# Optimization experiments

Measured on AMD Instinct MI355X. Metric: run time of the kernel, lower is better.

## Reference

```python
import jax, jax.numpy as jnp
import numpy as np

B, I, H = 32768, 1024, 1024

def _xavier(key, shape):
    fan_out, fan_in = shape
    limit = float(np.sqrt(6.0 / (fan_in + fan_out)))
    return jax.random.uniform(key, shape, jnp.float32, -limit, limit)

def setup_inputs() -> dict:
    key = jax.random.key(0)
    ks = jax.random.split(key, 8)
    return {
        "x": jax.random.normal(ks[0], (B, I), jnp.float32),
        "h": jax.random.normal(ks[1], (B, H), jnp.float32),
        "weight_ir": _xavier(ks[2], (H, I)),
        "weight_hr": _xavier(ks[3], (H, H)),
        "weight_iz": _xavier(ks[4], (H, I)),
        "weight_hz": _xavier(ks[5], (H, H)),
        "weight_in": _xavier(ks[6], (H, I)),
        "weight_hn": _xavier(ks[7], (H, H)),
        "bias_ir": jnp.zeros((H,), jnp.float32),
        "bias_hr": jnp.zeros((H,), jnp.float32),
        "bias_iz": jnp.zeros((H,), jnp.float32),
        "bias_hz": jnp.zeros((H,), jnp.float32),
        "bias_in": jnp.zeros((H,), jnp.float32),
        "bias_hn": jnp.zeros((H,), jnp.float32),
    }

def reference(x, h, weight_ir, weight_hr, weight_iz, weight_hz, weight_in, weight_hn,
              bias_ir, bias_hr, bias_iz, bias_hz, bias_in, bias_hn):
    # Fuse the 3 input-side and 3 hidden-side GEMMs into two concatenated GEMMs
    # (same math as 6 separate F.linear calls).
    Wi = jnp.concatenate([weight_ir, weight_iz, weight_in], axis=0)  # [3H, I]
    Wh = jnp.concatenate([weight_hr, weight_hz, weight_hn], axis=0)  # [3H, H]
    bi = jnp.concatenate([bias_ir, bias_iz, bias_in])
    bh = jnp.concatenate([bias_hr, bias_hz, bias_hn])
    gi = x @ Wi.T + bi   # [B, 3H]
    gh = h @ Wh.T + bh   # [B, 3H]
    Hd = weight_hr.shape[0]
    ir, iz, inn = gi[:, :Hd], gi[:, Hd:2*Hd], gi[:, 2*Hd:]
    hr, hz, hn = gh[:, :Hd], gh[:, Hd:2*Hd], gh[:, 2*Hd:]
    r = jax.nn.sigmoid(ir + hr)
    z = jax.nn.sigmoid(iz + hz)
    n = jnp.tanh(inn + r * hn)
    return (1.0 - z) * n + z * h
```

## Files before the change

kernel.cpp:

```cpp
#include <hip/hip_runtime.h>
#include <hip/hip_bf16.h>


#define B_ROWS 32768
#define KD     1024
#define HD     1024

#define BM 128
#define BN 64
#define BK 32

typedef __bf16 bf16_t;
typedef __bf16 bf16x8 __attribute__((ext_vector_type(8)));
typedef __bf16 bf16x4 __attribute__((ext_vector_type(4)));
typedef float  f32x4  __attribute__((ext_vector_type(4)));

#define XT_BYTES  67108864ull
#define WT_OFF   134217728ull
#define WS_NEEDED 146800640ull

#define X_SLOTS 4194304
#define W_BASE_SLOT 8388608
#define TOTAL_SLOTS 9175040

__device__ __forceinline__ float sigm_f(float v) { return 1.0f / (1.0f + __expf(-v)); }
__device__ __forceinline__ float tanh_f(float v) { return 2.0f / (1.0f + __expf(-2.0f * v)) - 1.0f; }

__device__ __forceinline__ bf16x4 cvt4(f32x4 v) {
    bf16x4 r;
    r[0] = (bf16_t)v[0]; r[1] = (bf16_t)v[1];
    r[2] = (bf16_t)v[2]; r[3] = (bf16_t)v[3];
    return r;
}

__device__ __forceinline__ void glds16(const void* g, void* l) {
    __builtin_amdgcn_global_load_lds(
        (const __attribute__((address_space(1))) void*)g,
        (__attribute__((address_space(3))) void*)l, 16, 0, 0);
}

struct WPtrs { const float* p[6]; };

__global__ void __launch_bounds__(256)
cvt_kernel(const float* __restrict__ x, const float* __restrict__ h,
           WPtrs wp, bf16_t* __restrict__ ws)
{
    int sid = blockIdx.x * 256 + threadIdx.x;
    if (sid >= TOTAL_SLOTS) return;

    const float* src;
    if (sid < W_BASE_SLOT) {
        const float* base = (sid < X_SLOTS) ? x : h;
        int s2   = sid & (X_SLOTS - 1);
        int tile = s2 >> 9;
        int c    = s2 & 511;
        int row  = c >> 2, s = c & 3;
        int mt   = tile >> 5, kt = tile & 31;
        int ks   = s ^ ((row >> 1) & 3);
        src = base + (size_t)(mt * 128 + row) * KD + kt * 32 + ks * 8;
    } else {
        int s2   = sid - W_BASE_SLOT;
        int tile = s2 / 1536;
        int c    = s2 % 1536;
        int g    = c >> 8;
        int cc   = c & 255;
        int row  = cc >> 2, s = cc & 3;
        int nt   = tile >> 5, kt = tile & 31;
        int ks   = s ^ ((row >> 1) & 3);
        src = wp.p[g] + (size_t)(nt * 64 + row) * KD + kt * 32 + ks * 8;
    }
    f32x4 a = *(const f32x4*)src;
    f32x4 b = *(const f32x4*)(src + 4);
    bf16x8 o;
    o[0]=(bf16_t)a[0]; o[1]=(bf16_t)a[1]; o[2]=(bf16_t)a[2]; o[3]=(bf16_t)a[3];
    o[4]=(bf16_t)b[0]; o[5]=(bf16_t)b[1]; o[6]=(bf16_t)b[2]; o[7]=(bf16_t)b[3];
    *(bf16x8*)(ws + (size_t)sid * 8) = o;
}

__global__ void __launch_bounds__(256, 2)
gru_mfma_kernel(const bf16_t* __restrict__ xt, const bf16_t* __restrict__ ht,
                const bf16_t* __restrict__ wt,
                const float* __restrict__ h,
                const float* __restrict__ b_ir, const float* __restrict__ b_hr,
                const float* __restrict__ b_iz, const float* __restrict__ b_hz,
                const float* __restrict__ b_in, const float* __restrict__ b_hn,
                float* __restrict__ out)
{
    __shared__ __align__(16) char smem[2][40960];

    const int tid  = threadIdx.x;
    const int lane = tid & 63;
    const int wid  = tid >> 6;
    const int wr   = wid >> 1;
    const int wc   = wid & 1;

    const int nblk = HD / BN;
    const int bidN = blockIdx.x % nblk;
    const int bidM = blockIdx.x / nblk;
    const int rowBase = bidM * BM;
    const int colBase = bidN * BN;

    const char* xcb = (const char*)xt + (size_t)bidM * 32 * 8192;
    const char* hcb = (const char*)ht + (size_t)bidM * 32 * 8192;
    const char* wcb = (const char*)wt + (size_t)bidN * 32 * 24576;

    const f32x4 vzero = {0.f, 0.f, 0.f, 0.f};
    f32x4 accR[4][2], accZ[4][2], accIN[4][2], accHN[4][2];
    #pragma unroll
    for (int m = 0; m < 4; ++m)
        #pragma unroll
        for (int n = 0; n < 2; ++n) {
            accR[m][n] = vzero; accZ[m][n] = vzero;
            accIN[m][n] = vzero; accHN[m][n] = vzero;
        }

    const int fr  = lane & 15;
    const int sl  = lane >> 4;
    const int f   = (fr >> 1) & 3;
    const int col = ((sl ^ f) << 4);
    int aoff[4], boff[2];
    #pragma unroll
    for (int m = 0; m < 4; ++m) aoff[m] = (wr * 64 + m * 16 + fr) * 64 + col;
    #pragma unroll
    for (int n = 0; n < 2; ++n) boff[n] = (wc * 32 + n * 16 + fr) * 64 + col;

    auto STAGE = [&](int buf, int kt) {
        const char* xc  = xcb + (size_t)kt * 8192;
        const char* hc  = hcb + (size_t)kt * 8192;
        const char* wc2 = wcb + (size_t)kt * 24576;
        char* s = smem[buf];
        #pragma unroll
        for (int i = 0; i < 2; ++i) {
            int off = wid * 2048 + i * 1024;
            glds16(xc + off + lane * 16, s + off);
            glds16(hc + off + lane * 16, s + 8192 + off);
        }
        #pragma unroll
        for (int j = 0; j < 6; ++j) {
            int off = wid * 6144 + j * 1024;
            glds16(wc2 + off + lane * 16, s + 16384 + off);
        }
    };

    auto COMPUTE = [&](const char* s) {
        bf16x8 xa[4], ha[4];
        #pragma unroll
        for (int m = 0; m < 4; ++m) {
            xa[m] = *(const bf16x8*)(s + aoff[m]);
            ha[m] = *(const bf16x8*)(s + 8192 + aoff[m]);
        }
        bf16x8 wb[6][2];
        #pragma unroll
        for (int g = 0; g < 6; ++g)
            #pragma unroll
            for (int n = 0; n < 2; ++n)
                wb[g][n] = *(const bf16x8*)(s + 16384 + g * 4096 + boff[n]);

        #pragma unroll
        for (int m = 0; m < 4; ++m) {
            #pragma unroll
            for (int n = 0; n < 2; ++n) {
                accR[m][n]  = __builtin_amdgcn_mfma_f32_16x16x32_bf16(xa[m], wb[0][n], accR[m][n], 0, 0, 0);
                accR[m][n]  = __builtin_amdgcn_mfma_f32_16x16x32_bf16(ha[m], wb[1][n], accR[m][n], 0, 0, 0);
                accZ[m][n]  = __builtin_amdgcn_mfma_f32_16x16x32_bf16(xa[m], wb[2][n], accZ[m][n], 0, 0, 0);
                accZ[m][n]  = __builtin_amdgcn_mfma_f32_16x16x32_bf16(ha[m], wb[3][n], accZ[m][n], 0, 0, 0);
                accIN[m][n] = __builtin_amdgcn_mfma_f32_16x16x32_bf16(xa[m], wb[4][n], accIN[m][n], 0, 0, 0);
                accHN[m][n] = __builtin_amdgcn_mfma_f32_16x16x32_bf16(ha[m], wb[5][n], accHN[m][n], 0, 0, 0);
            }
        }
    };

    STAGE(0, 0);

    for (int kt = 0; kt < 31; ++kt) {
        STAGE((kt + 1) & 1, kt + 1);
        asm volatile("s_waitcnt vmcnt(10)" ::: "memory");
        __builtin_amdgcn_s_barrier();
        __builtin_amdgcn_sched_barrier(0);
        COMPUTE(smem[kt & 1]);
        __builtin_amdgcn_sched_barrier(0);
        __builtin_amdgcn_s_barrier();
    }
    asm volatile("s_waitcnt vmcnt(0)" ::: "memory");
    __builtin_amdgcn_s_barrier();
    __builtin_amdgcn_sched_barrier(0);
    COMPUTE(smem[1]);

    const int rq = (lane >> 4) * 4;
    float br[2], bz[2], bi[2], bh[2];
    #pragma unroll
    for (int n = 0; n < 2; ++n) {
        int c = colBase + wc * 32 + n * 16 + fr;
        br[n] = b_ir[c] + b_hr[c];
        bz[n] = b_iz[c] + b_hz[c];
        bi[n] = b_in[c];
        bh[n] = b_hn[c];
    }
    #pragma unroll
    for (int m = 0; m < 4; ++m) {
        #pragma unroll
        for (int n = 0; n < 2; ++n) {
            int gc = colBase + wc * 32 + n * 16 + fr;
            #pragma unroll
            for (int j = 0; j < 4; ++j) {
                int gr = rowBase + wr * 64 + m * 16 + rq + j;
                float rv = sigm_f(accR[m][n][j] + br[n]);
                float zv = sigm_f(accZ[m][n][j] + bz[n]);
                float nv = tanh_f(accIN[m][n][j] + bi[n] + rv * (accHN[m][n][j] + bh[n]));
                float hv = h[(size_t)gr * HD + gc];
                out[(size_t)gr * HD + gc] = (1.0f - zv) * nv + zv * hv;
            }
        }
    }
}

#define PK 40
__global__ void __launch_bounds__(256, 2)
gru_fused_kernel(const float* __restrict__ x,  const float* __restrict__ h,
                 const float* __restrict__ w_ir, const float* __restrict__ w_hr,
                 const float* __restrict__ w_iz, const float* __restrict__ w_hz,
                 const float* __restrict__ w_in, const float* __restrict__ w_hn,
                 const float* __restrict__ b_ir, const float* __restrict__ b_hr,
                 const float* __restrict__ b_iz, const float* __restrict__ b_hz,
                 const float* __restrict__ b_in, const float* __restrict__ b_hn,
                 float* __restrict__ out)
{
    __shared__ __align__(16) bf16_t xs[BM][PK];
    __shared__ __align__(16) bf16_t hs[BM][PK];
    __shared__ __align__(16) bf16_t ws[6][BN][PK];

    const int tid  = threadIdx.x;
    const int lane = tid & 63;
    const int wid  = tid >> 6;
    const int wr   = wid >> 1;
    const int wc   = wid & 1;

    const int nblk = HD / BN;
    const int bidN = blockIdx.x % nblk;
    const int bidM = blockIdx.x / nblk;
    const int rowBase = bidM * BM;
    const int colBase = bidN * BN;

    const float* wptr[6] = { w_ir, w_hr, w_iz, w_hz, w_in, w_hn };

    int sr[4], sc[4];
    #pragma unroll
    for (int i = 0; i < 4; ++i) {
        int idx = tid + i * 256;
        sr[i] = idx >> 3;
        sc[i] = (idx & 7) * 4;
    }
    int xoff[4];
    #pragma unroll
    for (int i = 0; i < 4; ++i) xoff[i] = (rowBase + sr[i]) * KD + sc[i];
    int woff[2];
    #pragma unroll
    for (int i = 0; i < 2; ++i) woff[i] = (colBase + sr[i]) * KD + sc[i];

    const f32x4 vzero = {0.f, 0.f, 0.f, 0.f};
    f32x4 accR[4][2], accZ[4][2], accIN[4][2], accHN[4][2];
    #pragma unroll
    for (int m = 0; m < 4; ++m)
        #pragma unroll
        for (int n = 0; n < 2; ++n) {
            accR[m][n] = vzero; accZ[m][n] = vzero;
            accIN[m][n] = vzero; accHN[m][n] = vzero;
        }

    const int fr = lane & 15;
    const int ko = (lane >> 4) * 8;

    for (int k0 = 0; k0 < KD; k0 += BK) {
        __syncthreads();
        #pragma unroll
        for (int i = 0; i < 4; ++i) {
            f32x4 vx = *(const f32x4*)&x[xoff[i] + k0];
            f32x4 vh = *(const f32x4*)&h[xoff[i] + k0];
            *(bf16x4*)&xs[sr[i]][sc[i]] = cvt4(vx);
            *(bf16x4*)&hs[sr[i]][sc[i]] = cvt4(vh);
        }
        #pragma unroll
        for (int g = 0; g < 6; ++g) {
            #pragma unroll
            for (int i = 0; i < 2; ++i) {
                f32x4 vw = *(const f32x4*)&wptr[g][woff[i] + k0];
                *(bf16x4*)&ws[g][sr[i]][sc[i]] = cvt4(vw);
            }
        }
        __syncthreads();

        bf16x8 xa[4], ha[4];
        #pragma unroll
        for (int m = 0; m < 4; ++m) {
            xa[m] = *(const bf16x8*)&xs[wr * 64 + m * 16 + fr][ko];
            ha[m] = *(const bf16x8*)&hs[wr * 64 + m * 16 + fr][ko];
        }
        bf16x8 wb[6][2];
        #pragma unroll
        for (int g = 0; g < 6; ++g)
            #pragma unroll
            for (int n = 0; n < 2; ++n)
                wb[g][n] = *(const bf16x8*)&ws[g][wc * 32 + n * 16 + fr][ko];

        #pragma unroll
        for (int m = 0; m < 4; ++m) {
            #pragma unroll
            for (int n = 0; n < 2; ++n) {
                accR[m][n]  = __builtin_amdgcn_mfma_f32_16x16x32_bf16(xa[m], wb[0][n], accR[m][n], 0, 0, 0);
                accR[m][n]  = __builtin_amdgcn_mfma_f32_16x16x32_bf16(ha[m], wb[1][n], accR[m][n], 0, 0, 0);
                accZ[m][n]  = __builtin_amdgcn_mfma_f32_16x16x32_bf16(xa[m], wb[2][n], accZ[m][n], 0, 0, 0);
                accZ[m][n]  = __builtin_amdgcn_mfma_f32_16x16x32_bf16(ha[m], wb[3][n], accZ[m][n], 0, 0, 0);
                accIN[m][n] = __builtin_amdgcn_mfma_f32_16x16x32_bf16(xa[m], wb[4][n], accIN[m][n], 0, 0, 0);
                accHN[m][n] = __builtin_amdgcn_mfma_f32_16x16x32_bf16(ha[m], wb[5][n], accHN[m][n], 0, 0, 0);
            }
        }
    }

    const int rq = (lane >> 4) * 4;
    float br[2], bz[2], bi[2], bh[2];
    #pragma unroll
    for (int n = 0; n < 2; ++n) {
        int c = colBase + wc * 32 + n * 16 + fr;
        br[n] = b_ir[c] + b_hr[c];
        bz[n] = b_iz[c] + b_hz[c];
        bi[n] = b_in[c];
        bh[n] = b_hn[c];
    }
    #pragma unroll
    for (int m = 0; m < 4; ++m) {
        #pragma unroll
        for (int n = 0; n < 2; ++n) {
            int gc = colBase + wc * 32 + n * 16 + fr;
            #pragma unroll
            for (int j = 0; j < 4; ++j) {
                int gr = rowBase + wr * 64 + m * 16 + rq + j;
                float rv = sigm_f(accR[m][n][j] + br[n]);
                float zv = sigm_f(accZ[m][n][j] + bz[n]);
                float nv = tanh_f(accIN[m][n][j] + bi[n] + rv * (accHN[m][n][j] + bh[n]));
                float hv = h[gr * HD + gc];
                out[gr * HD + gc] = (1.0f - zv) * nv + zv * hv;
            }
        }
    }
}

extern "C" void kernel_launch(void* const* d_in, const int* in_sizes, int n_in,
                              void* d_out, int out_size, void* d_ws, size_t ws_size,
                              hipStream_t stream) {
    const float* x    = (const float*)d_in[0];
    const float* h    = (const float*)d_in[1];
    const float* w_ir = (const float*)d_in[2];
    const float* w_hr = (const float*)d_in[3];
    const float* w_iz = (const float*)d_in[4];
    const float* w_hz = (const float*)d_in[5];
    const float* w_in = (const float*)d_in[6];
    const float* w_hn = (const float*)d_in[7];
    const float* b_ir = (const float*)d_in[8];
    const float* b_hr = (const float*)d_in[9];
    const float* b_iz = (const float*)d_in[10];
    const float* b_hz = (const float*)d_in[11];
    const float* b_in = (const float*)d_in[12];
    const float* b_hn = (const float*)d_in[13];
    float* out = (float*)d_out;

    if (ws_size >= WS_NEEDED) {
        bf16_t* ws = (bf16_t*)d_ws;
        WPtrs wp;
        wp.p[0] = w_ir; wp.p[1] = w_hr; wp.p[2] = w_iz;
        wp.p[3] = w_hz; wp.p[4] = w_in; wp.p[5] = w_hn;
        cvt_kernel<<<(TOTAL_SLOTS + 255) / 256, 256, 0, stream>>>(x, h, wp, ws);

        const bf16_t* xt = ws;
        const bf16_t* ht = ws + XT_BYTES / 2;
        const bf16_t* wt = ws + WT_OFF / 2;
        dim3 grid((B_ROWS / BM) * (HD / BN));
        gru_mfma_kernel<<<grid, 256, 0, stream>>>(
            xt, ht, wt, h, b_ir, b_hr, b_iz, b_hz, b_in, b_hn, out);
    } else {
        dim3 grid((B_ROWS / BM) * (HD / BN));
        gru_fused_kernel<<<grid, 256, 0, stream>>>(
            x, h, w_ir, w_hr, w_iz, w_hz, w_in, w_hn,
            b_ir, b_hr, b_iz, b_hz, b_in, b_hn, out);
    }
}
```

Measured before the change: 473.2 us.

## Split K-step into three interleaved load/MFMA phases with priority and block swizzle

Reworks the main K loop so the next tile's global-to-LDS loads are spread across three compute phases (R, Z, N gates), each phase reading only its weight fragments from LDS before issuing MFMAs at raised wave priority. A block-index swizzle over 8 groups changes which M/N tiles run concurrently, aiming at better L2 reuse of the x/h and weight tiles. The goal is to overlap memory traffic with matrix math more finely. The cost is more barriers per iteration, and the vmcnt(4) wait in the loop looks like it may not cover the weight loads of the staged buffer.

```diff
diff --git a/kernel.cpp b/kernel.cpp
--- a/kernel.cpp
+++ b/kernel.cpp
@@ -94,9 +94,11 @@
     const int wr   = wid >> 1;
     const int wc   = wid & 1;
 
+    const int q    = gridDim.x >> 3;
+    const int swz  = (blockIdx.x & 7) * q + (blockIdx.x >> 3);
     const int nblk = HD / BN;
-    const int bidN = blockIdx.x % nblk;
-    const int bidM = blockIdx.x / nblk;
+    const int bidN = swz % nblk;
+    const int bidM = swz / nblk;
     const int rowBase = bidM * BM;
     const int colBase = bidN * BN;
 
@@ -124,7 +126,7 @@
     #pragma unroll
     for (int n = 0; n < 2; ++n) boff[n] = (wc * 32 + n * 16 + fr) * 64 + col;
 
-    auto STAGE = [&](int buf, int kt) {
+    auto STAGE_ALL = [&](int buf, int kt) {
         const char* xc  = xcb + (size_t)kt * 8192;
         const char* hc  = hcb + (size_t)kt * 8192;
         const char* wc2 = wcb + (size_t)kt * 24576;
@@ -142,22 +144,125 @@
         }
     };
 
-    auto COMPUTE = [&](const char* s) {
-        bf16x8 xa[4], ha[4];
+    STAGE_ALL(0, 0);
+
+    for (int kt = 0; kt < 31; ++kt) {
+        char* cur = smem[kt & 1];
+        char* nxt = smem[(kt + 1) & 1];
+        const char* xn = xcb + (size_t)(kt + 1) * 8192;
+        const char* hn = hcb + (size_t)(kt + 1) * 8192;
+        const char* wn = wcb + (size_t)(kt + 1) * 24576;
+
+        {
+            int off = wid * 2048;
+            glds16(xn + off + lane * 16,        nxt + off);
+            glds16(xn + off + 1024 + lane * 16, nxt + off + 1024);
+            glds16(hn + off + lane * 16,        nxt + 8192 + off);
+            glds16(hn + off + 1024 + lane * 16, nxt + 8192 + off + 1024);
+        }
+        asm volatile("s_waitcnt vmcnt(4)" ::: "memory");
+        __builtin_amdgcn_s_barrier();
+        __builtin_amdgcn_sched_barrier(0);
+
+        bf16x8 xa[4], ha[4], w0[2], w1[2];
         #pragma unroll
         for (int m = 0; m < 4; ++m) {
-            xa[m] = *(const bf16x8*)(s + aoff[m]);
-            ha[m] = *(const bf16x8*)(s + 8192 + aoff[m]);
-        }
-        bf16x8 wb[6][2];
+            xa[m] = *(const bf16x8*)(cur + aoff[m]);
+            ha[m] = *(const bf16x8*)(cur + 8192 + aoff[m]);
+        }
+        #pragma unroll
+        for (int n = 0; n < 2; ++n) {
+            w0[n] = *(const bf16x8*)(cur + 16384 + 0 * 4096 + boff[n]);
+            w1[n] = *(const bf16x8*)(cur + 16384 + 1 * 4096 + boff[n]);
+        }
+        #pragma unroll
+        for (int j = 0; j < 3; ++j) {
+            int off = wid * 6144 + j * 1024;
+            glds16(wn + off + lane * 16, nxt + 16384 + off);
+        }
+        __builtin_amdgcn_s_barrier();
+        asm volatile("s_waitcnt lgkmcnt(0)" ::: "memory");
+        __builtin_amdgcn_sched_barrier(0);
+        __builtin_amdgcn_s_setprio(1);
+        #pragma unroll
+        for (int m = 0; m < 4; ++m)
+            #pragma unroll
+            for (int n = 0; n < 2; ++n) {
+                accR[m][n] = __builtin_amdgcn_mfma_f32_16x16x32_bf16(xa[m], w0[n], accR[m][n], 0, 0, 0);
+                accR[m][n] = __builtin_amdgcn_mfma_f32_16x16x32_bf16(ha[m], w1[n], accR[m][n], 0, 0, 0);
+            }
+        __builtin_amdgcn_s_setprio(0);
+        __builtin_amdgcn_sched_barrier(0);
+        __builtin_amdgcn_s_barrier();
+
+        bf16x8 w2[2], w3[2];
+        #pragma unroll
+        for (int n = 0; n < 2; ++n) {
+            w2[n] = *(const bf16x8*)(cur + 16384 + 2 * 4096 + boff[n]);
+            w3[n] = *(const bf16x8*)(cur + 16384 + 3 * 4096 + boff[n]);
+        }
+        #pragma unroll
+        for (int j = 3; j < 6; ++j) {
+            int off = wid * 6144 + j * 1024;
+            glds16(wn + off + lane * 16, nxt + 16384 + off);
+        }
+        __builtin_amdgcn_s_barrier();
+        asm volatile("s_waitcnt lgkmcnt(0)" ::: "memory");
+        __builtin_amdgcn_sched_barrier(0);
+        __builtin_amdgcn_s_setprio(1);
+        #pragma unroll
+        for (int m = 0; m < 4; ++m)
+            #pragma unroll
+            for (int n = 0; n < 2; ++n) {
+                accZ[m][n] = __builtin_amdgcn_mfma_f32_16x16x32_bf16(xa[m], w2[n], accZ[m][n], 0, 0, 0);
+                accZ[m][n] = __builtin_amdgcn_mfma_f32_16x16x32_bf16(ha[m], w3[n], accZ[m][n], 0, 0, 0);
+            }
+        __builtin_amdgcn_s_setprio(0);
+        __builtin_amdgcn_sched_barrier(0);
+        __builtin_amdgcn_s_barrier();
+
+        bf16x8 w4[2], w5[2];
+        #pragma unroll
+        for (int n = 0; n < 2; ++n) {
+            w4[n] = *(const bf16x8*)(cur + 16384 + 4 * 4096 + boff[n]);
+            w5[n] = *(const bf16x8*)(cur + 16384 + 5 * 4096 + boff[n]);
+        }
+        __builtin_amdgcn_s_barrier();
+        asm volatile("s_waitcnt lgkmcnt(0)" ::: "memory");
+        __builtin_amdgcn_sched_barrier(0);
+        __builtin_amdgcn_s_setprio(1);
+        #pragma unroll
+        for (int m = 0; m < 4; ++m)
+            #pragma unroll
+            for (int n = 0; n < 2; ++n) {
+                accIN[m][n] = __builtin_amdgcn_mfma_f32_16x16x32_bf16(xa[m], w4[n], accIN[m][n], 0, 0, 0);
+                accHN[m][n] = __builtin_amdgcn_mfma_f32_16x16x32_bf16(ha[m], w5[n], accHN[m][n], 0, 0, 0);
+            }
+        __builtin_amdgcn_s_setprio(0);
+        __builtin_amdgcn_sched_barrier(0);
+        __builtin_amdgcn_s_barrier();
+    }
+
+    {
+        const char* cur = smem[1];
+        asm volatile("s_waitcnt vmcnt(0)" ::: "memory");
+        __builtin_amdgcn_s_barrier();
+        __builtin_amdgcn_sched_barrier(0);
+        bf16x8 xa[4], ha[4], wb[6][2];
+        #pragma unroll
+        for (int m = 0; m < 4; ++m) {
+            xa[m] = *(const bf16x8*)(cur + aoff[m]);
+            ha[m] = *(const bf16x8*)(cur + 8192 + aoff[m]);
+        }
         #pragma unroll
         for (int g = 0; g < 6; ++g)
             #pragma unroll
             for (int n = 0; n < 2; ++n)
-                wb[g][n] = *(const bf16x8*)(s + 16384 + g * 4096 + boff[n]);
-
-        #pragma unroll
-        for (int m = 0; m < 4; ++m) {
+                wb[g][n] = *(const bf16x8*)(cur + 16384 + g * 4096 + boff[n]);
+        asm volatile("s_waitcnt lgkmcnt(0)" ::: "memory");
+        __builtin_amdgcn_sched_barrier(0);
+        #pragma unroll
+        for (int m = 0; m < 4; ++m)
             #pragma unroll
             for (int n = 0; n < 2; ++n) {
                 accR[m][n]  = __builtin_amdgcn_mfma_f32_16x16x32_bf16(xa[m], wb[0][n], accR[m][n], 0, 0, 0);
@@ -167,24 +272,7 @@
                 accIN[m][n] = __builtin_amdgcn_mfma_f32_16x16x32_bf16(xa[m], wb[4][n], accIN[m][n], 0, 0, 0);
                 accHN[m][n] = __builtin_amdgcn_mfma_f32_16x16x32_bf16(ha[m], wb[5][n], accHN[m][n], 0, 0, 0);
             }
-        }
-    };
-
-    STAGE(0, 0);
-
-    for (int kt = 0; kt < 31; ++kt) {
-        STAGE((kt + 1) & 1, kt + 1);
-        asm volatile("s_waitcnt vmcnt(10)" ::: "memory");
-        __builtin_amdgcn_s_barrier();
-        __builtin_amdgcn_sched_barrier(0);
-        COMPUTE(smem[kt & 1]);
-        __builtin_amdgcn_sched_barrier(0);
-        __builtin_amdgcn_s_barrier();
-    }
-    asm volatile("s_waitcnt vmcnt(0)" ::: "memory");
-    __builtin_amdgcn_s_barrier();
-    __builtin_amdgcn_sched_barrier(0);
-    COMPUTE(smem[1]);
+    }
 
     const int rq = (lane >> 4) * 4;
     float br[2], bz[2], bi[2], bh[2];
```

New measurement: 492.5 us. 4.1% more time.

## Load A fragments directly from global into registers, stage only weights in LDS

Applied to the files above, without the earlier changes.

The cvt kernel now writes x and h in MFMA fragment order, so each lane can load its A operand straight from global memory into registers instead of routing it through LDS. Only the weight tiles are staged through shared memory, which cuts LDS use from 40 KB to 24 KB per buffer and removes the LDS reads for A. The k-loop is unrolled by two with ping-pong register fragments, and the vmcnt wait is raised to 14 to cover the extra in-flight loads. This adds register pressure, and the wait count must exactly match the number of outstanding loads to stay correct.

```diff
diff --git a/kernel.cpp b/kernel.cpp
--- a/kernel.cpp
+++ b/kernel.cpp
@@ -54,10 +54,13 @@
         int s2   = sid & (X_SLOTS - 1);
         int tile = s2 >> 9;
         int c    = s2 & 511;
-        int row  = c >> 2, s = c & 3;
+        int lane = c & 63;
+        int m    = (c >> 6) & 3;
+        int wrr  = c >> 8;
         int mt   = tile >> 5, kt = tile & 31;
-        int ks   = s ^ ((row >> 1) & 3);
-        src = base + (size_t)(mt * 128 + row) * KD + kt * 32 + ks * 8;
+        int row  = wrr * 64 + m * 16 + (lane & 15);
+        int kof  = (lane >> 4) * 8;
+        src = base + (size_t)(mt * 128 + row) * KD + kt * 32 + kof;
     } else {
         int s2   = sid - W_BASE_SLOT;
         int tile = s2 / 1536;
@@ -77,6 +80,8 @@
     *(bf16x8*)(ws + (size_t)sid * 8) = o;
 }
 
+struct Afrag { bf16x8 x0, x1, x2, x3, h0, h1, h2, h3; };
+
 __global__ void __launch_bounds__(256, 2)
 gru_mfma_kernel(const bf16_t* __restrict__ xt, const bf16_t* __restrict__ ht,
                 const bf16_t* __restrict__ wt,
@@ -86,7 +91,7 @@
                 const float* __restrict__ b_in, const float* __restrict__ b_hn,
                 float* __restrict__ out)
 {
-    __shared__ __align__(16) char smem[2][40960];
+    __shared__ __align__(16) char smem[2][24576];
 
     const int tid  = threadIdx.x;
     const int lane = tid & 63;
@@ -118,43 +123,44 @@
     const int sl  = lane >> 4;
     const int f   = (fr >> 1) & 3;
     const int col = ((sl ^ f) << 4);
-    int aoff[4], boff[2];
-    #pragma unroll
-    for (int m = 0; m < 4; ++m) aoff[m] = (wr * 64 + m * 16 + fr) * 64 + col;
+    int boff[2];
     #pragma unroll
     for (int n = 0; n < 2; ++n) boff[n] = (wc * 32 + n * 16 + fr) * 64 + col;
 
-    auto STAGE = [&](int buf, int kt) {
-        const char* xc  = xcb + (size_t)kt * 8192;
-        const char* hc  = hcb + (size_t)kt * 8192;
+    const int agof = wr * 4096 + lane * 16;
+
+    auto ALOAD = [&](Afrag& A, int kt) {
+        const char* xc = xcb + (size_t)kt * 8192 + agof;
+        const char* hc = hcb + (size_t)kt * 8192 + agof;
+        A.x0 = *(const bf16x8*)(xc);
+        A.x1 = *(const bf16x8*)(xc + 1024);
+        A.x2 = *(const bf16x8*)(xc + 2048);
+        A.x3 = *(const bf16x8*)(xc + 3072);
+        A.h0 = *(const bf16x8*)(hc);
+        A.h1 = *(const bf16x8*)(hc + 1024);
+        A.h2 = *(const bf16x8*)(hc + 2048);
+        A.h3 = *(const bf16x8*)(hc + 3072);
+    };
+
+    auto WSTAGE = [&](int buf, int kt) {
         const char* wc2 = wcb + (size_t)kt * 24576;
         char* s = smem[buf];
         #pragma unroll
-        for (int i = 0; i < 2; ++i) {
-            int off = wid * 2048 + i * 1024;
-            glds16(xc + off + lane * 16, s + off);
-            glds16(hc + off + lane * 16, s + 8192 + off);
-        }
-        #pragma unroll
         for (int j = 0; j < 6; ++j) {
             int off = wid * 6144 + j * 1024;
-            glds16(wc2 + off + lane * 16, s + 16384 + off);
+            glds16(wc2 + off + lane * 16, s + off);
         }
     };
 
-    auto COMPUTE = [&](const char* s) {
-        bf16x8 xa[4], ha[4];
-        #pragma unroll
-        for (int m = 0; m < 4; ++m) {
-            xa[m] = *(const bf16x8*)(s + aoff[m]);
-            ha[m] = *(const bf16x8*)(s + 8192 + aoff[m]);
-        }
+    auto COMPUTE = [&](const char* s, const Afrag& A) {
+        bf16x8 xa[4] = { A.x0, A.x1, A.x2, A.x3 };
+        bf16x8 ha[4] = { A.h0, A.h1, A.h2, A.h3 };
         bf16x8 wb[6][2];
         #pragma unroll
         for (int g = 0; g < 6; ++g)
             #pragma unroll
             for (int n = 0; n < 2; ++n)
-                wb[g][n] = *(const bf16x8*)(s + 16384 + g * 4096 + boff[n]);
+                wb[g][n] = *(const bf16x8*)(s + g * 4096 + boff[n]);
 
         #pragma unroll
         for (int m = 0; m < 4; ++m) {
@@ -170,21 +176,40 @@
         }
     };
 
-    STAGE(0, 0);
-
-    for (int kt = 0; kt < 31; ++kt) {
-        STAGE((kt + 1) & 1, kt + 1);
-        asm volatile("s_waitcnt vmcnt(10)" ::: "memory");
+    Afrag A0, A1;
+    ALOAD(A0, 0);
+    WSTAGE(0, 0);
+
+    for (int kt = 0; kt < 30; kt += 2) {
+        ALOAD(A1, kt + 1);
+        WSTAGE(1, kt + 1);
+        asm volatile("s_waitcnt vmcnt(14)" ::: "memory");
         __builtin_amdgcn_s_barrier();
         __builtin_amdgcn_sched_barrier(0);
-        COMPUTE(smem[kt & 1]);
+        COMPUTE(smem[0], A0);
         __builtin_amdgcn_sched_barrier(0);
         __builtin_amdgcn_s_barrier();
-    }
+        ALOAD(A0, kt + 2);
+        WSTAGE(0, kt + 2);
+        asm volatile("s_waitcnt vmcnt(14)" ::: "memory");
+        __builtin_amdgcn_s_barrier();
+        __builtin_amdgcn_sched_barrier(0);
+        COMPUTE(smem[1], A1);
+        __builtin_amdgcn_sched_barrier(0);
+        __builtin_amdgcn_s_barrier();
+    }
+    ALOAD(A1, 31);
+    WSTAGE(1, 31);
+    asm volatile("s_waitcnt vmcnt(14)" ::: "memory");
+    __builtin_amdgcn_s_barrier();
+    __builtin_amdgcn_sched_barrier(0);
+    COMPUTE(smem[0], A0);
+    __builtin_amdgcn_sched_barrier(0);
+    __builtin_amdgcn_s_barrier();
     asm volatile("s_waitcnt vmcnt(0)" ::: "memory");
     __builtin_amdgcn_s_barrier();
     __builtin_amdgcn_sched_barrier(0);
-    COMPUTE(smem[1]);
+    COMPUTE(smem[1], A1);
 
     const int rq = (lane >> 4) * 4;
     float br[2], bz[2], bi[2], bh[2];
```

After: 506.3 us. 1.07x slower.

## Load weight fragments directly from global into registers, bypassing LDS

Applied to the files above, without the earlier changes.

The weight pre-pack now lays out bf16 weights in MFMA fragment order per lane, so each wave reads its B operands straight from global memory into registers instead of staging them through shared memory. Only x and h tiles stay in LDS, which shrinks LDS per block from 80KB to 32KB and could allow more resident blocks. The cost is more global/L2 traffic per wave, because each wave with the same wc re-fetches weights, and a greater dependence on vmcnt ordering, since the weight loads are in flight alongside the async LDS copies.

```diff
diff --git a/kernel.cpp b/kernel.cpp
--- a/kernel.cpp
+++ b/kernel.cpp
@@ -64,10 +64,12 @@
         int c    = s2 % 1536;
         int g    = c >> 8;
         int cc   = c & 255;
-        int row  = cc >> 2, s = cc & 3;
+        int fq   = cc >> 6;
+        int lane = cc & 63;
         int nt   = tile >> 5, kt = tile & 31;
-        int ks   = s ^ ((row >> 1) & 3);
-        src = wp.p[g] + (size_t)(nt * 64 + row) * KD + kt * 32 + ks * 8;
+        int row  = fq * 16 + (lane & 15);
+        int kof  = (lane >> 4) * 8;
+        src = wp.p[g] + (size_t)(nt * 64 + row) * KD + kt * 32 + kof;
     }
     f32x4 a = *(const f32x4*)src;
     f32x4 b = *(const f32x4*)(src + 4);
@@ -86,7 +88,7 @@
                 const float* __restrict__ b_in, const float* __restrict__ b_hn,
                 float* __restrict__ out)
 {
-    __shared__ __align__(16) char smem[2][40960];
+    __shared__ __align__(16) char smem[2][16384];
 
     const int tid  = threadIdx.x;
     const int lane = tid & 63;
@@ -118,16 +120,15 @@
     const int sl  = lane >> 4;
     const int f   = (fr >> 1) & 3;
     const int col = ((sl ^ f) << 4);
-    int aoff[4], boff[2];
+    int aoff[4];
     #pragma unroll
     for (int m = 0; m < 4; ++m) aoff[m] = (wr * 64 + m * 16 + fr) * 64 + col;
-    #pragma unroll
-    for (int n = 0; n < 2; ++n) boff[n] = (wc * 32 + n * 16 + fr) * 64 + col;
+
+    const int wfo = wc * 2048 + lane * 16;
 
     auto STAGE = [&](int buf, int kt) {
-        const char* xc  = xcb + (size_t)kt * 8192;
-        const char* hc  = hcb + (size_t)kt * 8192;
-        const char* wc2 = wcb + (size_t)kt * 24576;
+        const char* xc = xcb + (size_t)kt * 8192;
+        const char* hc = hcb + (size_t)kt * 8192;
         char* s = smem[buf];
         #pragma unroll
         for (int i = 0; i < 2; ++i) {
@@ -135,27 +136,31 @@
             glds16(xc + off + lane * 16, s + off);
             glds16(hc + off + lane * 16, s + 8192 + off);
         }
-        #pragma unroll
-        for (int j = 0; j < 6; ++j) {
-            int off = wid * 6144 + j * 1024;
-            glds16(wc2 + off + lane * 16, s + 16384 + off);
-        }
     };
 
-    auto COMPUTE = [&](const char* s) {
+    STAGE(0, 0);
+
+    for (int kt = 0; kt < 31; ++kt) {
+        const char* wk = wcb + (size_t)kt * 24576 + wfo;
+        bf16x8 wb[6][2];
+        #pragma unroll
+        for (int g = 0; g < 6; ++g)
+            #pragma unroll
+            for (int n = 0; n < 2; ++n)
+                wb[g][n] = *(const bf16x8*)(wk + g * 4096 + n * 1024);
+
+        STAGE((kt + 1) & 1, kt + 1);
+        asm volatile("s_waitcnt vmcnt(16)" ::: "memory");
+        __builtin_amdgcn_s_barrier();
+        __builtin_amdgcn_sched_barrier(0);
+
+        const char* s = smem[kt & 1];
         bf16x8 xa[4], ha[4];
         #pragma unroll
         for (int m = 0; m < 4; ++m) {
             xa[m] = *(const bf16x8*)(s + aoff[m]);
             ha[m] = *(const bf16x8*)(s + 8192 + aoff[m]);
         }
-        bf16x8 wb[6][2];
-        #pragma unroll
-        for (int g = 0; g < 6; ++g)
-            #pragma unroll
-            for (int n = 0; n < 2; ++n)
-                wb[g][n] = *(const bf16x8*)(s + 16384 + g * 4096 + boff[n]);
-
         #pragma unroll
         for (int m = 0; m < 4; ++m) {
             #pragma unroll
@@ -168,23 +173,42 @@
                 accHN[m][n] = __builtin_amdgcn_mfma_f32_16x16x32_bf16(ha[m], wb[5][n], accHN[m][n], 0, 0, 0);
             }
         }
-    };
-
-    STAGE(0, 0);
-
-    for (int kt = 0; kt < 31; ++kt) {
-        STAGE((kt + 1) & 1, kt + 1);
-        asm volatile("s_waitcnt vmcnt(10)" ::: "memory");
+        __builtin_amdgcn_sched_barrier(0);
+        __builtin_amdgcn_s_barrier();
+    }
+
+    {
+        const int kt = 31;
+        const char* wk = wcb + (size_t)kt * 24576 + wfo;
+        bf16x8 wb[6][2];
+        #pragma unroll
+        for (int g = 0; g < 6; ++g)
+            #pragma unroll
+            for (int n = 0; n < 2; ++n)
+                wb[g][n] = *(const bf16x8*)(wk + g * 4096 + n * 1024);
+        asm volatile("s_waitcnt vmcnt(12)" ::: "memory");
         __builtin_amdgcn_s_barrier();
         __builtin_amdgcn_sched_barrier(0);
-        COMPUTE(smem[kt & 1]);
-        __builtin_amdgcn_sched_barrier(0);
-        __builtin_amdgcn_s_barrier();
-    }
-    asm volatile("s_waitcnt vmcnt(0)" ::: "memory");
-    __builtin_amdgcn_s_barrier();
-    __builtin_amdgcn_sched_barrier(0);
-    COMPUTE(smem[1]);
+        const char* s = smem[1];
+        bf16x8 xa[4], ha[4];
+        #pragma unroll
+        for (int m = 0; m < 4; ++m) {
+            xa[m] = *(const bf16x8*)(s + aoff[m]);
+            ha[m] = *(const bf16x8*)(s + 8192 + aoff[m]);
+        }
+        #pragma unroll
+        for (int m = 0; m < 4; ++m) {
+            #pragma unroll
+            for (int n = 0; n < 2; ++n) {
+                accR[m][n]  = __builtin_amdgcn_mfma_f32_16x16x32_bf16(xa[m], wb[0][n], accR[m][n], 0, 0, 0);
+                accR[m][n]  = __builtin_amdgcn_mfma_f32_16x16x32_bf16(ha[m], wb[1][n], accR[m][n], 0, 0, 0);
+                accZ[m][n]  = __builtin_amdgcn_mfma_f32_16x16x32_bf16(xa[m], wb[2][n], accZ[m][n], 0, 0, 0);
+                accZ[m][n]  = __builtin_amdgcn_mfma_f32_16x16x32_bf16(ha[m], wb[3][n], accZ[m][n], 0, 0, 0);
+                accIN[m][n] = __builtin_amdgcn_mfma_f32_16x16x32_bf16(xa[m], wb[4][n], accIN[m][n], 0, 0, 0);
+                accHN[m][n] = __builtin_amdgcn_mfma_f32_16x16x32_bf16(ha[m], wb[5][n], accHN[m][n], 0, 0, 0);
+            }
+        }
+    }
 
     const int rq = (lane >> 4) * 4;
     float br[2], bz[2], bi[2], bh[2];
```

Result: slower. 534.7 us (+13.0%).
